# Performance work log

Hardware: AMD Instinct MI355X
Metric: run time of the kernel (lower is better)

The kernel has to match this reference:

```python
import jax, jax.numpy as jnp
import numpy as np

# Model config (matches init_kwargs)
DATA_L = 256
LATENT_L = 64
LATENT_N = 8
N_COMPS = 8
LOG_2PI = float(np.log(2.0 * np.pi))


def setup_inputs() -> dict:
    key = jax.random.key(0)
    ks = jax.random.split(key, 7)
    B = 2048
    N = B * LATENT_N  # 16384
    x = jax.random.normal(ks[0], (B, DATA_L), dtype=jnp.float32)
    W_e = jax.random.normal(ks[1], (DATA_L, LATENT_L * N_COMPS * 3), dtype=jnp.float32) * 0.05
    b_e = jnp.zeros((LATENT_L * N_COMPS * 3,), dtype=jnp.float32)
    W_d = jax.random.normal(ks[2], (LATENT_L, DATA_L * N_COMPS * 3), dtype=jnp.float32) * 0.05
    b_d = jnp.zeros((DATA_L * N_COMPS * 3,), dtype=jnp.float32)
    u_e = jax.random.normal(ks[3], (N, LATENT_L), dtype=jnp.float32)
    r = jax.random.uniform(ks[4], (N, LATENT_L), dtype=jnp.float32)
    return {"x": x, "W_e": W_e, "b_e": b_e, "W_d": W_d, "b_d": b_d, "u_e": u_e, "r": r}


def _split3(pred, K, D):
    # pred: (N, 3*K*D) -> m, logp, loga each (N, K, D)
    m = pred[:, : K * D].reshape(-1, K, D)
    logp = pred[:, K * D : 2 * K * D].reshape(-1, K, D)
    loga = pred[:, 2 * K * D :].reshape(-1, K, D)
    loga = jax.nn.log_softmax(loga, axis=1)  # loga - logsumexp over comps
    return m, logp, loga


def _discrete_sample(loga, r):
    # loga: (N, K, D), r: (N, D). Matches torch: idx = sum((r > cumsum(p)).int(), dim=1)
    c = jnp.cumsum(jnp.exp(loga), axis=1)  # (N, K, D)
    idx = jnp.sum((r[:, None, :] > c).astype(jnp.int32), axis=1)  # (N, D)
    return jnp.clip(idx, 0, loga.shape[1] - 1)


def reference(x, W_e, b_e, W_d, b_d, u_e, r):
    K, L, D = N_COMPS, LATENT_L, DATA_L
    x_rep = jnp.tile(x, (LATENT_N, 1))  # (N, D)

    # Encoder (KAN with width=[data_l, 3*K*L] modeled as dense layer)
    pred_e = x_rep @ W_e + b_e  # (N, 3*K*L)
    m_e, logp_e, loga_e = _split3(pred_e, K, L)

    # Sample mixture component per (row, latent dim), gather, reparameterize
    idx = _discrete_sample(loga_e, r)  # (N, L) int32
    m_sel = jnp.take_along_axis(m_e, idx[:, None, :], axis=1)[:, 0, :]  # (N, L)
    logp_sel = jnp.take_along_axis(logp_e, idx[:, None, :], axis=1)[:, 0, :]
    h = m_sel + jnp.exp(-0.5 * logp_sel) * u_e  # (N, L)

    # log q(h|x): mixture-of-Gaussians density at h
    uh = jnp.exp(0.5 * logp_e) * (h[:, None, :] - m_e)  # (N, K, L)
    L_e = jax.nn.logsumexp(loga_e - 0.5 * uh * uh + 0.5 * logp_e, axis=1)  # (N, L)
    L_e = -0.5 * L * LOG_2PI + jnp.sum(L_e, axis=1)  # (N,)

    # log prior N(0, I)
    L_q = -0.5 * L * LOG_2PI - 0.5 * jnp.sum(h * h, axis=1)  # (N,)

    # Decoder mixture likelihood of x
    pred_d = h @ W_d + b_d  # (N, 3*K*D)
    m_d, logp_d, loga_d = _split3(pred_d, K, D)
    ux = jnp.exp(0.5 * logp_d) * (x_rep[:, None, :] - m_d)  # (N, K, D)
    L_d = jax.nn.logsumexp(loga_d - 0.5 * ux * ux + 0.5 * logp_d, axis=1)  # (N, D)
    L_d = -0.5 * D * LOG_2PI + jnp.sum(L_d, axis=1)  # (N,)

    return -jnp.mean(L_d + L_q - L_e)
```

## Files before the change

kernel.cpp:

```cpp
#include <hip/hip_runtime.h>
#include <hip/hip_bf16.h>
#include <math.h>

#define D_L   256
#define L_L   64
#define K_C   8
#define BATCH 2048
#define NTOT  16384
#define ENC_COLS 1536
#define LOG2PI 1.8378770664093453f
#define L2E    1.4426950408889634f
#define LN2    0.6931471805599453f
#define C_HL2E 0.7213475204444817f

typedef __attribute__((ext_vector_type(8)))  short short8;
typedef __attribute__((ext_vector_type(8)))  unsigned short ushort8;
typedef __attribute__((ext_vector_type(4)))  float float4_;
typedef __attribute__((ext_vector_type(16))) float float16_;

#if defined(__has_builtin)
#  if __has_builtin(__builtin_amdgcn_exp2f)
#    define EXP2F(x) __builtin_amdgcn_exp2f(x)
#  endif
#  if __has_builtin(__builtin_amdgcn_logf)
#    define LOG2F(x) __builtin_amdgcn_logf(x)
#  endif
#endif
#ifndef EXP2F
#  define EXP2F(x) __expf((x) * LN2)
#endif
#ifndef LOG2F
#  define LOG2F(x) (__logf(x) * L2E)
#endif

#define OFF_PE   0
#define OFF_H    (BATCH * ENC_COLS)
#define OFF_WET  (OFF_H + NTOT * L_L / 2)
#define OFF_WDT  (OFF_WET + ENC_COLS * D_L / 2)
#define OFF_ACC  (OFF_WDT + 6144 * 64 / 2)

__device__ __forceinline__ unsigned short f2bf(float f) {
  unsigned u = __float_as_uint(f);
  return (unsigned short)((u + 0x7fffu + ((u >> 16) & 1u)) >> 16);
}

__device__ __forceinline__ void gll16(const void* g, void* l) {
  __builtin_amdgcn_global_load_lds(
      (const __attribute__((address_space(1))) unsigned int*)g,
      (__attribute__((address_space(3))) unsigned int*)l, 16, 0, 0);
}

__global__ __launch_bounds__(256) void k_prep(
    const float* __restrict__ We, const float* __restrict__ Wd,
    unsigned short* __restrict__ WeT, unsigned short* __restrict__ WdT,
    float* __restrict__ accf)
{
  const int bid = blockIdx.x, t = threadIdx.x;
  if (bid < 96) {
    __shared__ float tile[64][65];
    const int cb = bid % 24, rb = bid / 24;
    const int c0 = cb * 64, r0 = rb * 64;
    {
      const int tr = t >> 2, tc = (t & 3) * 16;
      const float* src = We + (size_t)(r0 + tr) * ENC_COLS + c0 + tc;
      #pragma unroll
      for (int i = 0; i < 4; ++i) {
        float4_ v = *(const float4_*)(src + 4 * i);
        #pragma unroll
        for (int j = 0; j < 4; ++j) tile[tr][tc + 4 * i + j] = v[j];
      }
    }
    __syncthreads();
    const int c = t >> 2, ks = (t & 3) * 16;
    ushort8 o0, o1;
    #pragma unroll
    for (int j = 0; j < 8; ++j) {
      o0[j] = f2bf(tile[ks + j][c]);
      o1[j] = f2bf(tile[ks + 8 + j][c]);
    }
    unsigned short* dst = WeT + (size_t)(c0 + c) * D_L + r0 + ks;
    *(ushort8*)dst = o0;
    *(ushort8*)(dst + 8) = o1;
  } else if (bid < 192) {
    const int idx = bid - 96;
    const int comp = idx / 12, p = (idx % 12) >> 2, dt = idx & 3;
    const int c = t & 63, kg = t >> 6;
    const float scale = (p == 0) ? 1.0f : L2E;
    const float* src = Wd + (size_t)(kg * 16) * 6144 + p * 2048 + comp * 256 + dt * 64 + c;
    float v[16];
    #pragma unroll
    for (int i = 0; i < 16; ++i) v[i] = src[(size_t)i * 6144] * scale;
    unsigned short* base = WdT + ((((size_t)(comp * 3 + p) * 4 + dt) * 64 + c) << 6);
    #pragma unroll
    for (int j = 0; j < 2; ++j) {
      ushort8 o;
      #pragma unroll
      for (int e = 0; e < 8; ++e) o[e] = f2bf(v[j * 8 + e]);
      const int ch = (kg * 2 + j) ^ (c & 7);
      *(ushort8*)(base + ch * 8) = o;
    }
  } else {
    if (t == 0) accf[0] = 0.0f;
  }
}

__global__ __launch_bounds__(256) void k_enc(
    const float* __restrict__ x, const unsigned short* __restrict__ WeT,
    const float* __restrict__ be, float* __restrict__ pe)
{
  __shared__ __align__(16) unsigned short as_[64 * 72];
  __shared__ __align__(16) unsigned short bs_[64 * 72];
  const int t = threadIdx.x;
  const int w = t >> 6, l = t & 63;
  const int col = l & 31, q = l >> 5;
  const int rg = w >> 1, dg = w & 1;
  const int m0 = blockIdx.y * 64, c0 = blockIdx.x * 64;

  const float bias = be[c0 + dg * 32 + col];
  float16_ acc;
  #pragma unroll
  for (int e = 0; e < 16; ++e) acc[e] = bias;

  for (int kc = 0; kc < 4; ++kc) {
    if (kc) __syncthreads();
    #pragma unroll
    for (int p2 = 0; p2 < 2; ++p2) {
      const int ci = t + 256 * p2;
      const int row = ci >> 3, ch = ci & 7;
      const float* xs = x + (size_t)(m0 + row) * D_L + kc * 64 + ch * 8;
      float4_ v0 = *(const float4_*)xs;
      float4_ v1 = *(const float4_*)(xs + 4);
      ushort8 o;
      o[0] = f2bf(v0[0]); o[1] = f2bf(v0[1]); o[2] = f2bf(v0[2]); o[3] = f2bf(v0[3]);
      o[4] = f2bf(v1[0]); o[5] = f2bf(v1[1]); o[6] = f2bf(v1[2]); o[7] = f2bf(v1[3]);
      *(ushort8*)&as_[row * 72 + ch * 8] = o;
      *(ushort8*)&bs_[row * 72 + ch * 8] =
          *(const ushort8*)(WeT + (size_t)(c0 + row) * D_L + kc * 64 + ch * 8);
    }
    __syncthreads();
    const unsigned short* arow = &as_[(rg * 32 + col) * 72 + q * 8];
    const unsigned short* brow = &bs_[(dg * 32 + col) * 72 + q * 8];
    #pragma unroll
    for (int st = 0; st < 4; ++st) {
      short8 a = *(const short8*)(arow + st * 16);
      short8 b = *(const short8*)(brow + st * 16);
      acc = __builtin_amdgcn_mfma_f32_32x32x16_bf16(a, b, acc, 0, 0, 0);
    }
  }
  #pragma unroll
  for (int e = 0; e < 16; ++e) {
    const int row = (e & 3) + 8 * (e >> 2) + 4 * q;
    pe[(size_t)(m0 + rg * 32 + row) * ENC_COLS + c0 + dg * 32 + col] = acc[e];
  }
}

__global__ __launch_bounds__(256) void k_enc_post(
    const float* __restrict__ pe, const float* __restrict__ ue,
    const float* __restrict__ rr, unsigned short* __restrict__ h,
    float* __restrict__ accf)
{
  const int lane = threadIdx.x & 63;
  const int w = threadIdx.x >> 6;
  const int b = blockIdx.x * 4 + w;
  const float* row = pe + (size_t)b * ENC_COLS + lane;

  float m[8], p[8], a[8];
  #pragma unroll
  for (int k = 0; k < K_C; ++k) {
    m[k] = row[k * 64]; p[k] = row[512 + k * 64]; a[k] = row[1024 + k * 64];
  }
  float amax = a[0];
  #pragma unroll
  for (int k = 1; k < K_C; ++k) amax = fmaxf(amax, a[k]);
  float sa = 0.f;
  #pragma unroll
  for (int k = 0; k < K_C; ++k) sa += __expf(a[k] - amax);
  const float lse_a = amax + __logf(sa);

  float cum[8];
  {
    float cs = 0.f;
    #pragma unroll
    for (int k = 0; k < K_C; ++k) { cs += __expf(a[k] - lse_a); cum[k] = cs; }
  }
  float ep[8];
  #pragma unroll
  for (int k = 0; k < K_C; ++k) ep[k] = __expf(p[k]);

  const int sw = ((((lane >> 3) ^ (b & 7)) << 3) | (lane & 7));

  float tot = 0.f;
  for (int j = 0; j < 8; ++j) {
    const int n = b + BATCH * j;
    const float rv = rr[(size_t)n * L_L + lane];
    const float uv = ue[(size_t)n * L_L + lane];
    int idx = 0;
    #pragma unroll
    for (int k = 0; k < K_C; ++k) idx += (rv > cum[k]) ? 1 : 0;
    idx = min(idx, K_C - 1);
    float msel = m[0], psel = p[0];
    #pragma unroll
    for (int k = 1; k < K_C; ++k) {
      const bool sel = (idx == k);
      msel = sel ? m[k] : msel;
      psel = sel ? p[k] : psel;
    }
    const float hv = fmaf(__expf(-0.5f * psel), uv, msel);
    h[(size_t)n * L_L + sw] = f2bf(hv);

    float st = 0.f;
    #pragma unroll
    for (int k = 0; k < K_C; ++k) {
      const float dd = hv - m[k];
      const float tt = a[k] + 0.5f * p[k] - 0.5f * ep[k] * dd * dd;
      st += __expf(tt);
    }
    tot += -0.5f * hv * hv - (__logf(st + 1e-30f) - lse_a);
  }
  #pragma unroll
  for (int off = 1; off < 64; off <<= 1) tot += __shfl_xor(tot, off, 64);
  __shared__ float red2[4];
  if (lane == 0) red2[w] = tot;
  __syncthreads();
  if (threadIdx.x == 0) atomicAdd(accf, red2[0] + red2[1] + red2[2] + red2[3]);
}

__global__ __launch_bounds__(256, 2) void k_dec(
    const unsigned short* __restrict__ hb, const float* __restrict__ x,
    const unsigned short* __restrict__ WdT, const float* __restrict__ bd,
    float* __restrict__ accf)
{
  __shared__ __align__(16) unsigned short hs[128 * 64];
  __shared__ __align__(16) unsigned short bT[2][3 * 64 * 64];
  __shared__ float biasLds[1536];

  const int t = threadIdx.x;
  const int w = t >> 6, l = t & 63;
  const int col = l & 31, q = l >> 5, c7 = col & 7;
  const int rg = w >> 1, dg = w & 1;
  const int dt = blockIdx.x, d0 = dt * 64;
  const int n0 = blockIdx.y * 128;

  {
    const char* hg = (const char*)hb + (size_t)n0 * 128;
    #pragma unroll
    for (int j = 0; j < 4; ++j) {
      const int cj = (w << 2) | j;
      gll16(hg + cj * 1024 + l * 16, (char*)hs + cj * 1024);
    }
  }
  #pragma unroll
  for (int p = 0; p < 3; ++p) {
    const char* gsrc = (const char*)WdT + (((size_t)p * 4 + dt) << 13);
    #pragma unroll
    for (int j = 0; j < 2; ++j) {
      const int cj = (w << 1) | j;
      gll16(gsrc + cj * 1024 + l * 16, (char*)bT[0] + p * 8192 + cj * 1024);
    }
  }
  #pragma unroll
  for (int i = 0; i < 6; ++i) {
    const int idx = t + 256 * i;
    const int pp = idx >> 9, comp = (idx >> 6) & 7, d = idx & 63;
    float v = bd[pp * 2048 + comp * 256 + d0 + d];
    if (pp) v *= L2E;
    biasLds[idx] = v;
  }
  float xv[2][16];
  #pragma unroll
  for (int t2 = 0; t2 < 2; ++t2)
    #pragma unroll
    for (int e = 0; e < 16; ++e) {
      const int rw = (e & 3) + 8 * (e >> 2) + 4 * q;
      const int n = n0 + t2 * 64 + rg * 32 + rw;
      xv[t2][e] = x[(size_t)(n & (BATCH - 1)) * D_L + d0 + dg * 32 + col];
    }

  __syncthreads();

  short8 af[2][4];
  #pragma unroll
  for (int t2 = 0; t2 < 2; ++t2)
    #pragma unroll
    for (int st = 0; st < 4; ++st) {
      const int ch = ((st * 2 + q) ^ c7);
      af[t2][st] = *(const short8*)((const char*)hs + t2 * 8192 +
                                    (rg * 32 + col) * 128 + ch * 16);
    }

  float s_a[2][16], s_t[2][16];
  #pragma unroll
  for (int t2 = 0; t2 < 2; ++t2)
    #pragma unroll
    for (int e = 0; e < 16; ++e) { s_a[t2][e] = 0.f; s_t[t2][e] = 0.f; }

  const int browoff = (dg * 32 + col) * 128;

  for (int kc = 0; kc < K_C; ++kc) {
    if (kc < 7) {
      #pragma unroll
      for (int p = 0; p < 3; ++p) {
        const char* gsrc = (const char*)WdT + (((size_t)((kc + 1) * 3 + p) * 4 + dt) << 13);
        #pragma unroll
        for (int j = 0; j < 2; ++j) {
          const int cj = (w << 1) | j;
          gll16(gsrc + cj * 1024 + l * 16,
                (char*)bT[(kc + 1) & 1] + p * 8192 + cj * 1024);
        }
      }
    }
    const float bm = biasLds[kc * 64 + dg * 32 + col];
    const float bp = biasLds[512 + kc * 64 + dg * 32 + col];
    const float ba = biasLds[1024 + kc * 64 + dg * 32 + col];
    const char* bbuf = (const char*)bT[kc & 1];

    #pragma unroll
    for (int t2 = 0; t2 < 2; ++t2) {
      float16_ am, ap, aa;
      #pragma unroll
      for (int e = 0; e < 16; ++e) { am[e] = bm; ap[e] = bp; aa[e] = ba; }
      #pragma unroll
      for (int st = 0; st < 4; ++st) {
        const int ch = ((st * 2 + q) ^ c7) * 16;
        short8 wm_ = *(const short8*)(bbuf + browoff + ch);
        short8 wp_ = *(const short8*)(bbuf + 8192 + browoff + ch);
        short8 wa_ = *(const short8*)(bbuf + 16384 + browoff + ch);
        am = __builtin_amdgcn_mfma_f32_32x32x16_bf16(af[t2][st], wm_, am, 0, 0, 0);
        ap = __builtin_amdgcn_mfma_f32_32x32x16_bf16(af[t2][st], wp_, ap, 0, 0, 0);
        aa = __builtin_amdgcn_mfma_f32_32x32x16_bf16(af[t2][st], wa_, aa, 0, 0, 0);
      }
      #pragma unroll
      for (int e = 0; e < 16; ++e) {
        const float dd = xv[t2][e] - am[e];
        const float ex2 = EXP2F(ap[e]);
        const float t1 = fmaf(0.5f, ap[e], aa[e]);
        const float ttL = fmaf(-C_HL2E * ex2, dd * dd, t1);
        s_a[t2][e] += EXP2F(aa[e]);
        s_t[t2][e] += EXP2F(ttL);
      }
    }
    __syncthreads();
  }

  float v = 0.f;
  #pragma unroll
  for (int t2 = 0; t2 < 2; ++t2)
    #pragma unroll
    for (int e = 0; e < 16; ++e)
      v += LOG2F(s_t[t2][e] + 1e-30f) - LOG2F(s_a[t2][e]);
  v *= LN2;
  #pragma unroll
  for (int off = 1; off < 64; off <<= 1) v += __shfl_xor(v, off, 64);
  float* red = (float*)hs;
  if (l == 0) red[w] = v;
  __syncthreads();
  if (t == 0) atomicAdd(accf, red[0] + red[1] + red[2] + red[3]);
}

__global__ void k_final(const float* __restrict__ accf, float* __restrict__ out)
{
  if (threadIdx.x == 0) out[0] = -(accf[0] / (float)NTOT) + 128.0f * LOG2PI;
}

extern "C" void kernel_launch(void* const* d_in, const int* in_sizes, int n_in,
                              void* d_out, int out_size, void* d_ws, size_t ws_size,
                              hipStream_t stream)
{
  const float* x  = (const float*)d_in[0];
  const float* We = (const float*)d_in[1];
  const float* be = (const float*)d_in[2];
  const float* Wd = (const float*)d_in[3];
  const float* bd = (const float*)d_in[4];
  const float* ue = (const float*)d_in[5];
  const float* rr = (const float*)d_in[6];
  float* out = (float*)d_out;

  float* ws = (float*)d_ws;
  float* pe           = ws + OFF_PE;
  unsigned short* h   = (unsigned short*)(ws + OFF_H);
  unsigned short* WeT = (unsigned short*)(ws + OFF_WET);
  unsigned short* WdT = (unsigned short*)(ws + OFF_WDT);
  float* accf         = ws + OFF_ACC;

  k_prep<<<dim3(193), 256, 0, stream>>>(We, Wd, WeT, WdT, accf);
  k_enc<<<dim3(ENC_COLS / 64, BATCH / 64), 256, 0, stream>>>(x, WeT, be, pe);
  k_enc_post<<<dim3(BATCH / 4), 256, 0, stream>>>(pe, ue, rr, h, accf);
  k_dec<<<dim3(4, NTOT / 128), 256, 0, stream>>>(h, x, WdT, bd, accf);
  k_final<<<dim3(1), 64, 0, stream>>>(accf, out);
}
```

Before: 134.1 us.

## Pre-swizzle weights and h into MFMA fragment order, drop LDS staging in GEMMs

The prep kernel now writes encoder and decoder weights directly in per-lane MFMA fragment order, and the encoder-post kernel writes h in the same fragment layout. This lets the decoder and encoder load B (and A for the decoder) fragments straight from global memory into registers, with no LDS, no async global-to-LDS copies and no per-chunk barriers. The decoder tile shrinks from 128 to 64 rows, doubling the grid, and bias is added after the MFMA instead of being preloaded. The cost is that every wave re-reads weight fragments from global/L2 instead of sharing them through LDS, so global traffic goes up.

```diff
diff --git a/kernel.cpp b/kernel.cpp
--- a/kernel.cpp
+++ b/kernel.cpp
@@ -15,6 +15,7 @@
 
 typedef __attribute__((ext_vector_type(8)))  short short8;
 typedef __attribute__((ext_vector_type(8)))  unsigned short ushort8;
+typedef __attribute__((ext_vector_type(4)))  unsigned short ushort4_;
 typedef __attribute__((ext_vector_type(4)))  float float4_;
 typedef __attribute__((ext_vector_type(16))) float float16_;
 
@@ -33,117 +34,99 @@
 #  define LOG2F(x) (__logf(x) * L2E)
 #endif
 
-#define OFF_PE   0
-#define OFF_H    (BATCH * ENC_COLS)
-#define OFF_WET  (OFF_H + NTOT * L_L / 2)
-#define OFF_WDT  (OFF_WET + ENC_COLS * D_L / 2)
-#define OFF_ACC  (OFF_WDT + 6144 * 64 / 2)
+#define OFF_PE    0
+#define OFF_H     (BATCH * ENC_COLS)
+#define OFF_WET2  (OFF_H + NTOT * L_L / 2)
+#define OFF_WDT2  (OFF_WET2 + ENC_COLS * D_L / 2)
+#define OFF_ACC   (OFF_WDT2 + 6144 * 64 / 2)
 
 __device__ __forceinline__ unsigned short f2bf(float f) {
   unsigned u = __float_as_uint(f);
   return (unsigned short)((u + 0x7fffu + ((u >> 16) & 1u)) >> 16);
 }
 
-__device__ __forceinline__ void gll16(const void* g, void* l) {
-  __builtin_amdgcn_global_load_lds(
-      (const __attribute__((address_space(1))) unsigned int*)g,
-      (__attribute__((address_space(3))) unsigned int*)l, 16, 0, 0);
-}
-
 __global__ __launch_bounds__(256) void k_prep(
     const float* __restrict__ We, const float* __restrict__ Wd,
-    unsigned short* __restrict__ WeT, unsigned short* __restrict__ WdT,
+    unsigned short* __restrict__ WeT2, unsigned short* __restrict__ WdT2,
     float* __restrict__ accf)
 {
   const int bid = blockIdx.x, t = threadIdx.x;
+  if (bid == 192) { if (t == 0) accf[0] = 0.0f; return; }
+
+  const float* src; int C, rowbase, colbase; float scale;
+  unsigned short* dst;
   if (bid < 96) {
-    __shared__ float tile[64][65];
-    const int cb = bid % 24, rb = bid / 24;
-    const int c0 = cb * 64, r0 = rb * 64;
-    {
-      const int tr = t >> 2, tc = (t & 3) * 16;
-      const float* src = We + (size_t)(r0 + tr) * ENC_COLS + c0 + tc;
-      #pragma unroll
-      for (int i = 0; i < 4; ++i) {
-        float4_ v = *(const float4_*)(src + 4 * i);
-        #pragma unroll
-        for (int j = 0; j < 4; ++j) tile[tr][tc + 4 * i + j] = v[j];
-      }
-    }
-    __syncthreads();
-    const int c = t >> 2, ks = (t & 3) * 16;
-    ushort8 o0, o1;
-    #pragma unroll
-    for (int j = 0; j < 8; ++j) {
-      o0[j] = f2bf(tile[ks + j][c]);
-      o1[j] = f2bf(tile[ks + 8 + j][c]);
-    }
-    unsigned short* dst = WeT + (size_t)(c0 + c) * D_L + r0 + ks;
-    *(ushort8*)dst = o0;
-    *(ushort8*)(dst + 8) = o1;
-  } else if (bid < 192) {
+    const int comp = bid / 12, p = (bid % 12) >> 2, dt = bid & 3;
+    src = Wd; C = 6144; rowbase = 0;
+    colbase = p * 2048 + comp * 256 + dt * 64;
+    scale = p ? L2E : 1.0f;
+    dst = WdT2 + (size_t)bid * 4096;
+  } else {
     const int idx = bid - 96;
-    const int comp = idx / 12, p = (idx % 12) >> 2, dt = idx & 3;
-    const int c = t & 63, kg = t >> 6;
-    const float scale = (p == 0) ? 1.0f : L2E;
-    const float* src = Wd + (size_t)(kg * 16) * 6144 + p * 2048 + comp * 256 + dt * 64 + c;
-    float v[16];
-    #pragma unroll
-    for (int i = 0; i < 16; ++i) v[i] = src[(size_t)i * 6144] * scale;
-    unsigned short* base = WdT + ((((size_t)(comp * 3 + p) * 4 + dt) * 64 + c) << 6);
-    #pragma unroll
-    for (int j = 0; j < 2; ++j) {
-      ushort8 o;
-      #pragma unroll
-      for (int e = 0; e < 8; ++e) o[e] = f2bf(v[j * 8 + e]);
-      const int ch = (kg * 2 + j) ^ (c & 7);
-      *(ushort8*)(base + ch * 8) = o;
-    }
-  } else {
-    if (t == 0) accf[0] = 0.0f;
+    src = We; C = ENC_COLS; rowbase = (idx & 3) * 64;
+    colbase = (idx >> 2) * 64;
+    scale = 1.0f;
+    dst = WeT2 + (size_t)idx * 4096;
+  }
+
+  __shared__ float tile[64][65];
+  {
+    const int col = t & 63, w0 = t >> 6;
+    #pragma unroll
+    for (int i = 0; i < 16; ++i) {
+      const int r = w0 + i * 4;
+      tile[r][col] = src[(size_t)(rowbase + r) * C + colbase + col] * scale;
+    }
+  }
+  __syncthreads();
+  const int st = t >> 6, q = (t >> 5) & 1, c = t & 31;
+  #pragma unroll
+  for (int dg = 0; dg < 2; ++dg) {
+    ushort8 o;
+    #pragma unroll
+    for (int j = 0; j < 8; ++j) o[j] = f2bf(tile[st * 16 + q * 8 + j][dg * 32 + c]);
+    *(ushort8*)(dst + ((((size_t)dg * 4 + st) * 2 + q) * 32 + c) * 8) = o;
   }
 }
 
 __global__ __launch_bounds__(256) void k_enc(
-    const float* __restrict__ x, const unsigned short* __restrict__ WeT,
+    const float* __restrict__ x, const unsigned short* __restrict__ WeT2,
     const float* __restrict__ be, float* __restrict__ pe)
 {
-  __shared__ __align__(16) unsigned short as_[64 * 72];
-  __shared__ __align__(16) unsigned short bs_[64 * 72];
+  __shared__ __align__(16) unsigned short as_[64 * 264];
   const int t = threadIdx.x;
   const int w = t >> 6, l = t & 63;
   const int col = l & 31, q = l >> 5;
   const int rg = w >> 1, dg = w & 1;
-  const int m0 = blockIdx.y * 64, c0 = blockIdx.x * 64;
+  const int m0 = blockIdx.y * 64, cblk = blockIdx.x, c0 = cblk * 64;
+
+  {
+    const int kc4 = (t & 63) * 4;
+    #pragma unroll
+    for (int i = 0; i < 16; ++i) {
+      const int r = (t >> 6) + i * 4;
+      float4_ v = *(const float4_*)(x + (size_t)(m0 + r) * D_L + kc4);
+      ushort4_ o;
+      o[0] = f2bf(v[0]); o[1] = f2bf(v[1]); o[2] = f2bf(v[2]); o[3] = f2bf(v[3]);
+      *(ushort4_*)&as_[r * 264 + kc4] = o;
+    }
+  }
 
   const float bias = be[c0 + dg * 32 + col];
   float16_ acc;
   #pragma unroll
   for (int e = 0; e < 16; ++e) acc[e] = bias;
 
+  __syncthreads();
+
+  const unsigned short* arow = &as_[(rg * 32 + col) * 264 + q * 8];
+  const unsigned short* bbase = WeT2 + (size_t)cblk * 16384 + dg * 2048 + l * 8;
+  #pragma unroll
   for (int kc = 0; kc < 4; ++kc) {
-    if (kc) __syncthreads();
-    #pragma unroll
-    for (int p2 = 0; p2 < 2; ++p2) {
-      const int ci = t + 256 * p2;
-      const int row = ci >> 3, ch = ci & 7;
-      const float* xs = x + (size_t)(m0 + row) * D_L + kc * 64 + ch * 8;
-      float4_ v0 = *(const float4_*)xs;
-      float4_ v1 = *(const float4_*)(xs + 4);
-      ushort8 o;
-      o[0] = f2bf(v0[0]); o[1] = f2bf(v0[1]); o[2] = f2bf(v0[2]); o[3] = f2bf(v0[3]);
-      o[4] = f2bf(v1[0]); o[5] = f2bf(v1[1]); o[6] = f2bf(v1[2]); o[7] = f2bf(v1[3]);
-      *(ushort8*)&as_[row * 72 + ch * 8] = o;
-      *(ushort8*)&bs_[row * 72 + ch * 8] =
-          *(const ushort8*)(WeT + (size_t)(c0 + row) * D_L + kc * 64 + ch * 8);
-    }
-    __syncthreads();
-    const unsigned short* arow = &as_[(rg * 32 + col) * 72 + q * 8];
-    const unsigned short* brow = &bs_[(dg * 32 + col) * 72 + q * 8];
     #pragma unroll
     for (int st = 0; st < 4; ++st) {
-      short8 a = *(const short8*)(arow + st * 16);
-      short8 b = *(const short8*)(brow + st * 16);
+      short8 a = *(const short8*)(arow + kc * 64 + st * 16);
+      short8 b = *(const short8*)(bbase + (size_t)kc * 4096 + st * 512);
       acc = __builtin_amdgcn_mfma_f32_32x32x16_bf16(a, b, acc, 0, 0, 0);
     }
   }
@@ -187,7 +170,7 @@
   #pragma unroll
   for (int k = 0; k < K_C; ++k) ep[k] = __expf(p[k]);
 
-  const int sw = ((((lane >> 3) ^ (b & 7)) << 3) | (lane & 7));
+  const int st = lane >> 4, qq = (lane >> 3) & 1, jj = lane & 7;
 
   float tot = 0.f;
   for (int j = 0; j < 8; ++j) {
@@ -206,16 +189,18 @@
       psel = sel ? p[k] : psel;
     }
     const float hv = fmaf(__expf(-0.5f * psel), uv, msel);
-    h[(size_t)n * L_L + sw] = f2bf(hv);
-
-    float st = 0.f;
+
+    const int nblk = n >> 6, rgn = (n >> 5) & 1, coln = n & 31;
+    h[((((size_t)(nblk * 2 + rgn) * 4 + st) * 2 + qq) * 32 + coln) * 8 + jj] = f2bf(hv);
+
+    float stt = 0.f;
     #pragma unroll
     for (int k = 0; k < K_C; ++k) {
       const float dd = hv - m[k];
       const float tt = a[k] + 0.5f * p[k] - 0.5f * ep[k] * dd * dd;
-      st += __expf(tt);
-    }
-    tot += -0.5f * hv * hv - (__logf(st + 1e-30f) - lse_a);
+      stt += __expf(tt);
+    }
+    tot += -0.5f * hv * hv - (__logf(stt + 1e-30f) - lse_a);
   }
   #pragma unroll
   for (int off = 1; off < 64; off <<= 1) tot += __shfl_xor(tot, off, 64);
@@ -226,132 +211,79 @@
 }
 
 __global__ __launch_bounds__(256, 2) void k_dec(
-    const unsigned short* __restrict__ hb, const float* __restrict__ x,
-    const unsigned short* __restrict__ WdT, const float* __restrict__ bd,
+    const unsigned short* __restrict__ hF, const float* __restrict__ x,
+    const unsigned short* __restrict__ WdT2, const float* __restrict__ bd,
     float* __restrict__ accf)
 {
-  __shared__ __align__(16) unsigned short hs[128 * 64];
-  __shared__ __align__(16) unsigned short bT[2][3 * 64 * 64];
-  __shared__ float biasLds[1536];
-
   const int t = threadIdx.x;
   const int w = t >> 6, l = t & 63;
-  const int col = l & 31, q = l >> 5, c7 = col & 7;
+  const int col = l & 31, q = l >> 5;
   const int rg = w >> 1, dg = w & 1;
   const int dt = blockIdx.x, d0 = dt * 64;
-  const int n0 = blockIdx.y * 128;
-
-  {
-    const char* hg = (const char*)hb + (size_t)n0 * 128;
-    #pragma unroll
-    for (int j = 0; j < 4; ++j) {
-      const int cj = (w << 2) | j;
-      gll16(hg + cj * 1024 + l * 16, (char*)hs + cj * 1024);
-    }
-  }
-  #pragma unroll
-  for (int p = 0; p < 3; ++p) {
-    const char* gsrc = (const char*)WdT + (((size_t)p * 4 + dt) << 13);
-    #pragma unroll
-    for (int j = 0; j < 2; ++j) {
-      const int cj = (w << 1) | j;
-      gll16(gsrc + cj * 1024 + l * 16, (char*)bT[0] + p * 8192 + cj * 1024);
-    }
-  }
-  #pragma unroll
-  for (int i = 0; i < 6; ++i) {
-    const int idx = t + 256 * i;
-    const int pp = idx >> 9, comp = (idx >> 6) & 7, d = idx & 63;
-    float v = bd[pp * 2048 + comp * 256 + d0 + d];
-    if (pp) v *= L2E;
-    biasLds[idx] = v;
-  }
-  float xv[2][16];
-  #pragma unroll
-  for (int t2 = 0; t2 < 2; ++t2)
+  const int nblk = blockIdx.y, n0 = nblk * 64;
+  const int colD = d0 + dg * 32 + col;
+
+  const unsigned short* hbase = hF + ((size_t)(nblk * 2 + rg) * 4) * 512 + l * 8;
+  short8 af[4];
+  #pragma unroll
+  for (int st = 0; st < 4; ++st) af[st] = *(const short8*)(hbase + st * 512);
+
+  float xv[16];
+  #pragma unroll
+  for (int e = 0; e < 16; ++e) {
+    const int rw = (e & 3) + 8 * (e >> 2) + 4 * q;
+    const int n = n0 + rg * 32 + rw;
+    xv[e] = x[(size_t)(n & (BATCH - 1)) * D_L + colD];
+  }
+
+  float s_a[16], s_t[16];
+  #pragma unroll
+  for (int e = 0; e < 16; ++e) { s_a[e] = 0.f; s_t[e] = 0.f; }
+
+  const unsigned short* wbase = WdT2 + dg * 2048 + l * 8;
+
+  for (int comp = 0; comp < K_C; ++comp) {
+    const float bm  = bd[comp * 256 + colD];
+    const float bpL = bd[2048 + comp * 256 + colD] * L2E;
+    const float baL = bd[4096 + comp * 256 + colD] * L2E;
+
+    short8 bf[3][4];
+    #pragma unroll
+    for (int p = 0; p < 3; ++p) {
+      const unsigned short* pb = wbase + ((size_t)(comp * 3 + p) * 4 + dt) * 4096;
+      #pragma unroll
+      for (int st = 0; st < 4; ++st) bf[p][st] = *(const short8*)(pb + st * 512);
+    }
+
+    float16_ am = {}, ap = {}, aa = {};
+    #pragma unroll
+    for (int st = 0; st < 4; ++st) {
+      am = __builtin_amdgcn_mfma_f32_32x32x16_bf16(af[st], bf[0][st], am, 0, 0, 0);
+      ap = __builtin_amdgcn_mfma_f32_32x32x16_bf16(af[st], bf[1][st], ap, 0, 0, 0);
+      aa = __builtin_amdgcn_mfma_f32_32x32x16_bf16(af[st], bf[2][st], aa, 0, 0, 0);
+    }
+
     #pragma unroll
     for (int e = 0; e < 16; ++e) {
-      const int rw = (e & 3) + 8 * (e >> 2) + 4 * q;
-      const int n = n0 + t2 * 64 + rg * 32 + rw;
-      xv[t2][e] = x[(size_t)(n & (BATCH - 1)) * D_L + d0 + dg * 32 + col];
-    }
-
-  __syncthreads();
-
-  short8 af[2][4];
-  #pragma unroll
-  for (int t2 = 0; t2 < 2; ++t2)
-    #pragma unroll
-    for (int st = 0; st < 4; ++st) {
-      const int ch = ((st * 2 + q) ^ c7);
-      af[t2][st] = *(const short8*)((const char*)hs + t2 * 8192 +
-                                    (rg * 32 + col) * 128 + ch * 16);
-    }
-
-  float s_a[2][16], s_t[2][16];
-  #pragma unroll
-  for (int t2 = 0; t2 < 2; ++t2)
-    #pragma unroll
-    for (int e = 0; e < 16; ++e) { s_a[t2][e] = 0.f; s_t[t2][e] = 0.f; }
-
-  const int browoff = (dg * 32 + col) * 128;
-
-  for (int kc = 0; kc < K_C; ++kc) {
-    if (kc < 7) {
-      #pragma unroll
-      for (int p = 0; p < 3; ++p) {
-        const char* gsrc = (const char*)WdT + (((size_t)((kc + 1) * 3 + p) * 4 + dt) << 13);
-        #pragma unroll
-        for (int j = 0; j < 2; ++j) {
-          const int cj = (w << 1) | j;
-          gll16(gsrc + cj * 1024 + l * 16,
-                (char*)bT[(kc + 1) & 1] + p * 8192 + cj * 1024);
-        }
-      }
-    }
-    const float bm = biasLds[kc * 64 + dg * 32 + col];
-    const float bp = biasLds[512 + kc * 64 + dg * 32 + col];
-    const float ba = biasLds[1024 + kc * 64 + dg * 32 + col];
-    const char* bbuf = (const char*)bT[kc & 1];
-
-    #pragma unroll
-    for (int t2 = 0; t2 < 2; ++t2) {
-      float16_ am, ap, aa;
-      #pragma unroll
-      for (int e = 0; e < 16; ++e) { am[e] = bm; ap[e] = bp; aa[e] = ba; }
-      #pragma unroll
-      for (int st = 0; st < 4; ++st) {
-        const int ch = ((st * 2 + q) ^ c7) * 16;
-        short8 wm_ = *(const short8*)(bbuf + browoff + ch);
-        short8 wp_ = *(const short8*)(bbuf + 8192 + browoff + ch);
-        short8 wa_ = *(const short8*)(bbuf + 16384 + browoff + ch);
-        am = __builtin_amdgcn_mfma_f32_32x32x16_bf16(af[t2][st], wm_, am, 0, 0, 0);
-        ap = __builtin_amdgcn_mfma_f32_32x32x16_bf16(af[t2][st], wp_, ap, 0, 0, 0);
-        aa = __builtin_amdgcn_mfma_f32_32x32x16_bf16(af[t2][st], wa_, aa, 0, 0, 0);
-      }
-      #pragma unroll
-      for (int e = 0; e < 16; ++e) {
-        const float dd = xv[t2][e] - am[e];
-        const float ex2 = EXP2F(ap[e]);
-        const float t1 = fmaf(0.5f, ap[e], aa[e]);
-        const float ttL = fmaf(-C_HL2E * ex2, dd * dd, t1);
-        s_a[t2][e] += EXP2F(aa[e]);
-        s_t[t2][e] += EXP2F(ttL);
-      }
-    }
-    __syncthreads();
+      const float dd  = xv[e] - (am[e] + bm);
+      const float lpL = ap[e] + bpL;
+      const float laL = aa[e] + baL;
+      const float ex2 = EXP2F(lpL);
+      const float t1  = fmaf(0.5f, lpL, laL);
+      const float ttL = fmaf(-C_HL2E * ex2, dd * dd, t1);
+      s_a[e] += EXP2F(laL);
+      s_t[e] += EXP2F(ttL);
+    }
   }
 
   float v = 0.f;
   #pragma unroll
-  for (int t2 = 0; t2 < 2; ++t2)
-    #pragma unroll
-    for (int e = 0; e < 16; ++e)
-      v += LOG2F(s_t[t2][e] + 1e-30f) - LOG2F(s_a[t2][e]);
+  for (int e = 0; e < 16; ++e)
+    v += LOG2F(s_t[e] + 1e-30f) - LOG2F(s_a[e]);
   v *= LN2;
   #pragma unroll
   for (int off = 1; off < 64; off <<= 1) v += __shfl_xor(v, off, 64);
-  float* red = (float*)hs;
+  __shared__ float red[4];
   if (l == 0) red[w] = v;
   __syncthreads();
   if (t == 0) atomicAdd(accf, red[0] + red[1] + red[2] + red[3]);
@@ -376,15 +308,15 @@
   float* out = (float*)d_out;
 
   float* ws = (float*)d_ws;
-  float* pe           = ws + OFF_PE;
-  unsigned short* h   = (unsigned short*)(ws + OFF_H);
-  unsigned short* WeT = (unsigned short*)(ws + OFF_WET);
-  unsigned short* WdT = (unsigned short*)(ws + OFF_WDT);
-  float* accf         = ws + OFF_ACC;
-
-  k_prep<<<dim3(193), 256, 0, stream>>>(We, Wd, WeT, WdT, accf);
-  k_enc<<<dim3(ENC_COLS / 64, BATCH / 64), 256, 0, stream>>>(x, WeT, be, pe);
+  float* pe            = ws + OFF_PE;
+  unsigned short* h    = (unsigned short*)(ws + OFF_H);
+  unsigned short* WeT2 = (unsigned short*)(ws + OFF_WET2);
+  unsigned short* WdT2 = (unsigned short*)(ws + OFF_WDT2);
+  float* accf          = ws + OFF_ACC;
+
+  k_prep<<<dim3(193), 256, 0, stream>>>(We, Wd, WeT2, WdT2, accf);
+  k_enc<<<dim3(ENC_COLS / 64, BATCH / 64), 256, 0, stream>>>(x, WeT2, be, pe);
   k_enc_post<<<dim3(BATCH / 4), 256, 0, stream>>>(pe, ue, rr, h, accf);
-  k_dec<<<dim3(4, NTOT / 128), 256, 0, stream>>>(h, x, WdT, bd, accf);
+  k_dec<<<dim3(4, NTOT / 64), 256, 0, stream>>>(h, x, WdT2, bd, accf);
   k_final<<<dim3(1), 64, 0, stream>>>(accf, out);
 }
```

Result: faster. 123.8 us (-7.7%).
